# Kernel optimization log

Measured on AMD Instinct MI355X. Metric: run time of the kernel, lower is better.

## Reference

```python
import jax, jax.numpy as jnp
import numpy as np

B, S = 2, 1024
ENC_IN, MARK_IN = 21, 4
PRED_LEN, C_OUT = 96, 21
E = 512                 # embedding_dim
INNER = 2 * E           # proj_factor=2.0 (library default; Model does not pass it)
NH = 8                  # mLSTM heads
DH = INNER // NH        # 128
K = 4                   # causal conv1d kernel
BS = 4                  # qkv_proj_blocksize
NHP = INNER // BS       # 256 block-diagonal proj heads
NB = 4                  # num_blocks
EPS = 1e-5


def setup_inputs() -> dict:
    key = jax.random.key(0)
    ks = jax.random.split(key, 24)
    it = iter(range(24))
    def n(shape, s=0.02):
        return jax.random.normal(ks[next(it)], shape, jnp.float32) * s
    return {
        "x_enc": n((B, S, ENC_IN), 1.0),
        "x_mark_enc": n((B, S, MARK_IN), 1.0),
        "x_dec": n((B, PRED_LEN, ENC_IN), 1.0),
        "x_mark_dec": n((B, PRED_LEN, MARK_IN), 1.0),
        "emb_W": n((ENC_IN + MARK_IN, E), 0.05),
        "emb_b": jnp.zeros((E,), jnp.float32),
        "ln_w": jnp.ones((NB, E), jnp.float32),
        "up_W": n((NB, E, 2 * INNER)),
        "conv_W": n((NB, INNER, K), 0.1),
        "conv_b": jnp.zeros((NB, INNER), jnp.float32),
        "q_W": n((NB, NHP, BS, BS), 0.1),
        "k_W": n((NB, NHP, BS, BS), 0.1),
        "v_W": n((NB, NHP, BS, BS), 0.1),
        "ig_W": n((NB, 3 * INNER, NH)),
        "ig_b": jnp.zeros((NB, NH), jnp.float32),
        "fg_W": n((NB, 3 * INNER, NH)),
        "fg_b": jnp.tile(jnp.linspace(3.0, 6.0, NH, dtype=jnp.float32), (NB, 1)),
        "skip": jnp.ones((NB, INNER), jnp.float32),
        "onorm_w": jnp.ones((NB, INNER), jnp.float32),
        "down_W": n((NB, INNER, E)),
        "post_ln_w": jnp.ones((E,), jnp.float32),
        "head_W": n((E, C_OUT), 0.05),
        "head_b": jnp.zeros((C_OUT,), jnp.float32),
    }


def _ln(x, w):
    mu = jnp.mean(x, -1, keepdims=True)
    var = jnp.var(x, -1, keepdims=True)
    return (x - mu) * jax.lax.rsqrt(var + EPS) * w


def _headwise(x, w):
    # block-diagonal LinearHeadwiseExpand: (B,S,INNER) with (NHP,BS,BS) blocks
    xh = x.reshape(x.shape[0], x.shape[1], NHP, BS)
    return jnp.einsum('bshd,hod->bsho', xh, w).reshape(x.shape)


def _block(x, lw, uW, cW, cb, qW, kW, vW, igW, igb, fgW, fgb, sk, ow, dW):
    xn = _ln(x, lw)
    up = xn @ uW                                  # (B,S,2*INNER)
    xm, z = up[..., :INNER], up[..., INNER:]
    # causal depthwise conv1d + SiLU
    xc = jax.lax.conv_general_dilated(
        xm.transpose(0, 2, 1), cW[:, None, :], (1,), [(K - 1, 0)],
        feature_group_count=INNER,
        dimension_numbers=('NCH', 'OIH', 'NCH')).transpose(0, 2, 1) + cb
    xc = jax.nn.silu(xc)
    q = _headwise(xc, qW)
    k = _headwise(xc, kW)
    v = _headwise(xm, vW)
    qkv = jnp.concatenate([q, k, v], -1)          # (B,S,3*INNER)
    ig = (qkv @ igW + igb).transpose(0, 2, 1)     # (B,NH,S)
    fg = (qkv @ fgW + fgb).transpose(0, 2, 1)
    qh = q.reshape(B, S, NH, DH).transpose(0, 2, 1, 3)
    kh = k.reshape(B, S, NH, DH).transpose(0, 2, 1, 3)
    vh = v.reshape(B, S, NH, DH).transpose(0, 2, 1, 3)
    # parallel stabilized mLSTM (exp-gated linear attention)
    log_f = jax.nn.log_sigmoid(fg)
    cs = jnp.cumsum(log_f, -1)                    # (B,NH,S)
    Mmat = cs[..., :, None] - cs[..., None, :]    # (B,NH,S,S) cumulative decay
    tri = jnp.tril(jnp.ones((S, S), bool))
    logD = jnp.where(tri, Mmat + ig[..., None, :], -jnp.inf)
    m = jnp.max(logD, -1, keepdims=True)          # row-wise stabilizer
    D = jnp.exp(logD - m)
    qk = jnp.einsum('bnsd,bntd->bnst', qh, kh) / (DH ** 0.5)
    C = qk * D
    norm = jnp.maximum(jnp.abs(jnp.sum(C, -1, keepdims=True)), jnp.exp(-m))
    h = jnp.einsum('bnst,bntd->bnsd', C / (norm + 1e-6), vh)
    # multi-head layernorm (groupnorm over DH per head), weight, no bias
    hn = (h - jnp.mean(h, -1, keepdims=True)) * jax.lax.rsqrt(jnp.var(h, -1, keepdims=True) + EPS)
    hn = hn.transpose(0, 2, 1, 3).reshape(B, S, INNER) * ow
    hs = (hn + sk * xc) * jax.nn.silu(z)          # learnable skip + output gate
    return x + hs @ dW                            # residual


def reference(x_enc, x_mark_enc, x_dec, x_mark_dec, emb_W, emb_b, ln_w, up_W,
              conv_W, conv_b, q_W, k_W, v_W, ig_W, ig_b, fg_W, fg_b, skip,
              onorm_w, down_W, post_ln_w, head_W, head_b):
    x = jnp.concatenate([x_enc, x_mark_enc], -1) @ emb_W + emb_b
    for i in range(NB):
        x = _block(x, ln_w[i], up_W[i], conv_W[i], conv_b[i], q_W[i], k_W[i],
                   v_W[i], ig_W[i], ig_b[i], fg_W[i], fg_b[i], skip[i],
                   onorm_w[i], down_W[i])
    x = _ln(x, post_ln_w)
    return x[:, -PRED_LEN:, :] @ head_W + head_b
```

## Files before the change

### kernel.cpp

```cpp
#include <hip/hip_runtime.h>
#include <hip/hip_bf16.h>

#define S_LEN 1024
#define E_DIM 512
#define INNER_D 1024
#define NHEAD 8
#define DHEAD 128

typedef unsigned short u16;
typedef unsigned int u32;
typedef __attribute__((ext_vector_type(8))) short short8;
typedef __attribute__((ext_vector_type(4))) float f32x4;

union S8 { short8 v; u16 u[8]; uint4 q; };

__device__ __forceinline__ u16 f2bf(float f) {
  u32 u = __float_as_uint(f);
  u32 r = u + 0x7FFFu + ((u >> 16) & 1u);
  return (u16)(r >> 16);
}
__device__ __forceinline__ float bf2f(u16 u) { return __uint_as_float(((u32)u) << 16); }

__device__ __forceinline__ void gload16(const u16* g, u16* l) {
  __builtin_amdgcn_global_load_lds((const __attribute__((address_space(1))) void*)g,
                                   (__attribute__((address_space(3))) void*)l, 16, 0, 0);
}

__global__ __launch_bounds__(128) void embed_kernel(
    const float* __restrict__ xe, const float* __restrict__ xm,
    const float* __restrict__ W, const float* __restrict__ bias,
    float* __restrict__ x)
{
  int row = blockIdx.x;
  int tid = threadIdx.x;
  __shared__ float in_s[25];
  if (tid < 21) in_s[tid] = xe[row * 21 + tid];
  else if (tid < 25) in_s[tid] = xm[row * 4 + tid - 21];
  __syncthreads();
#pragma unroll
  for (int rep = 0; rep < 4; rep++) {
    int e = tid + rep * 128;
    float acc = bias[e];
#pragma unroll
    for (int i = 0; i < 25; i++) acc += in_s[i] * W[i * E_DIM + e];
    x[(size_t)row * E_DIM + e] = acc;
  }
}

__global__ __launch_bounds__(256) void ln_kernel(
    const float* __restrict__ x, const float* __restrict__ w, u16* __restrict__ out)
{
  int row = blockIdx.x, tid = threadIdx.x;
  const float* xr = x + (size_t)row * E_DIM;
  float2 v = *(const float2*)(xr + tid * 2);
  float s = v.x + v.y, q = v.x * v.x + v.y * v.y;
#pragma unroll
  for (int off = 32; off; off >>= 1) { s += __shfl_xor(s, off); q += __shfl_xor(q, off); }
  __shared__ float ssum[4], ssq[4];
  int wv = tid >> 6;
  if ((tid & 63) == 0) { ssum[wv] = s; ssq[wv] = q; }
  __syncthreads();
  s = ssum[0] + ssum[1] + ssum[2] + ssum[3];
  q = ssq[0] + ssq[1] + ssq[2] + ssq[3];
  float mu = s * (1.f / E_DIM);
  float var = q * (1.f / E_DIM) - mu * mu;
  float rs = rsqrtf(var + 1e-5f);
  int e = tid * 2;
  ushort2 o;
  o.x = f2bf((v.x - mu) * rs * w[e]);
  o.y = f2bf((v.y - mu) * rs * w[e + 1]);
  *(ushort2*)(out + (size_t)row * E_DIM + e) = o;
}

__global__ __launch_bounds__(256) void lnhead_kernel(
    const float* __restrict__ x, const float* __restrict__ w,
    const float* __restrict__ hW, const float* __restrict__ hb,
    float* __restrict__ out)
{
  int ridx = blockIdx.x;
  int b = ridx / 96, r = ridx % 96;
  int row = b * S_LEN + (S_LEN - 96) + r;
  int tid = threadIdx.x;
  const float* xr = x + (size_t)row * E_DIM;
  float2 v = *(const float2*)(xr + tid * 2);
  float s = v.x + v.y, q = v.x * v.x + v.y * v.y;
#pragma unroll
  for (int off = 32; off; off >>= 1) { s += __shfl_xor(s, off); q += __shfl_xor(q, off); }
  __shared__ float ssum[4], ssq[4];
  __shared__ float lnv[512];
  __shared__ float part[8][32];
  int wv = tid >> 6;
  if ((tid & 63) == 0) { ssum[wv] = s; ssq[wv] = q; }
  __syncthreads();
  s = ssum[0] + ssum[1] + ssum[2] + ssum[3];
  q = ssq[0] + ssq[1] + ssq[2] + ssq[3];
  float mu = s * (1.f / E_DIM);
  float var = q * (1.f / E_DIM) - mu * mu;
  float rs = rsqrtf(var + 1e-5f);
  int e = tid * 2;
  lnv[e]     = (v.x - mu) * rs * w[e];
  lnv[e + 1] = (v.y - mu) * rs * w[e + 1];
  __syncthreads();
  int n = tid & 31, sl = tid >> 5;
  float p = 0.f;
  if (n < 21) {
#pragma unroll 8
    for (int kk = 0; kk < 64; kk++)
      p += lnv[sl * 64 + kk] * hW[(sl * 64 + kk) * 21 + n];
  }
  part[sl][n] = p;
  __syncthreads();
  if (tid < 21) {
    float acc = hb[tid];
#pragma unroll
    for (int j = 0; j < 8; j++) acc += part[j][tid];
    out[ridx * 21 + tid] = acc;
  }
}

__global__ __launch_bounds__(256) void transpose_bf16_all_kernel(
    const float* __restrict__ in0, u16* __restrict__ out0, int K, int N)
{
  __shared__ u16 T[64][72];
  int L = blockIdx.z;
  const float* in = in0 + (size_t)L * K * N;
  u16* out = out0 + (size_t)L * N * K;
  int k0 = blockIdx.x * 64, n0 = blockIdx.y * 64;
  int t = threadIdx.x;
  int kr = t >> 2, nseg = (t & 3) * 16;
  const float* src = in + (size_t)(k0 + kr) * N + n0 + nseg;
#pragma unroll
  for (int j = 0; j < 16; j++) T[kr][nseg + j] = f2bf(src[j]);
  __syncthreads();
  int nr = t >> 2, kseg = (t & 3) * 16;
  u32 u[8];
#pragma unroll
  for (int rr = 0; rr < 8; rr++) {
    u32 lo = T[kseg + 2 * rr][nr];
    u32 hi = T[kseg + 2 * rr + 1][nr];
    u[rr] = lo | (hi << 16);
  }
  u16* dst = out + (size_t)(n0 + nr) * K + k0 + kseg;
  uint4 w0 = {u[0], u[1], u[2], u[3]};
  uint4 w1 = {u[4], u[5], u[6], u[7]};
  *(uint4*)dst = w0;
  *(uint4*)(dst + 8) = w1;
}

__global__ __launch_bounds__(256) void gates_w_transpose_kernel(
    const float* __restrict__ igW, const float* __restrict__ fgW,
    u16* __restrict__ hi, u16* __restrict__ lo)
{
  int L = blockIdx.z;
  int n = blockIdx.y;
  int k = blockIdx.x * 256 + threadIdx.x;
  const float* W = ((n < 8) ? igW : fgW) + (size_t)L * 24576;
  float v = W[(size_t)k * 8 + (n & 7)];
  u16 h = f2bf(v);
  u16 l = f2bf(v - bf2f(h));
  size_t o = ((size_t)L * 16 + n) * 3072 + k;
  hi[o] = h;
  lo[o] = l;
}

__global__ __launch_bounds__(256) void gemm_bf16_split64(
    const u16* __restrict__ A, const u16* __restrict__ Bt,
    float* __restrict__ C0, u16* __restrict__ C1,
    int M, int N, int K, int split_col, int ldc)
{
  __shared__ u16 As0[64 * 64], As1[64 * 64];
  __shared__ u16 Bs0[128 * 64], Bs1[128 * 64];
  const int tid = threadIdx.x;
  const int row0 = blockIdx.y * 64, col0 = blockIdx.x * 128;
  const int wave = tid >> 6, lane = tid & 63;
  const int wr = wave >> 1, wc = wave & 1;
  const int lm = lane & 15, lq = lane >> 4;
  const int lr = lane >> 3;
  const int cg = (lane & 7) ^ lr;
  f32x4 acc[2][4] = {};
  const u16* Abase = A + (size_t)(row0 + lr) * K + cg * 8;
  const u16* Bbase = Bt + (size_t)(col0 + lr) * K + cg * 8;
  const int key = lm & 7;

#define STAGE_UP(AS, BS, K0) do { \
  _Pragma("unroll") for (int i = 0; i < 2; i++) \
    gload16(Abase + (size_t)((wave * 2 + i) * 8) * K + (K0), &AS[(wave * 2 + i) * 512]); \
  _Pragma("unroll") for (int j = 0; j < 4; j++) \
    gload16(Bbase + (size_t)((wave * 4 + j) * 8) * K + (K0), &BS[(wave * 4 + j) * 512]); \
} while (0)

#define COMPUTE_UP(AS, BS) do { \
  short8 af[2][2], bfv[2][4]; \
  _Pragma("unroll") for (int kc = 0; kc < 2; kc++) { \
    _Pragma("unroll") for (int i = 0; i < 2; i++) \
      af[kc][i] = *(const short8*)&AS[(wr * 32 + i * 16 + lm) * 64 + (((kc * 4 + lq) ^ key) * 8)]; \
    _Pragma("unroll") for (int j = 0; j < 4; j++) \
      bfv[kc][j] = *(const short8*)&BS[(wc * 64 + j * 16 + lm) * 64 + (((kc * 4 + lq) ^ key) * 8)]; \
  } \
  _Pragma("unroll") for (int kc = 0; kc < 2; kc++) \
    _Pragma("unroll") for (int i = 0; i < 2; i++) \
      _Pragma("unroll") for (int j = 0; j < 4; j++) \
        acc[i][j] = __builtin_amdgcn_mfma_f32_16x16x32_bf16(af[kc][i], bfv[kc][j], acc[i][j], 0, 0, 0); \
} while (0)

  STAGE_UP(As0, Bs0, 0);
  STAGE_UP(As1, Bs1, 64);
#pragma unroll
  for (int t = 0; t < 8; t++) {
    if (t < 7) asm volatile("s_waitcnt vmcnt(6)" ::: "memory");
    else       asm volatile("s_waitcnt vmcnt(0)" ::: "memory");
    __builtin_amdgcn_sched_barrier(0);
    __builtin_amdgcn_s_barrier();
    if (t & 1) COMPUTE_UP(As1, Bs1); else COMPUTE_UP(As0, Bs0);
    __builtin_amdgcn_s_barrier();
    if (t + 2 < 8) {
      if (t & 1) STAGE_UP(As1, Bs1, (t + 2) * 64);
      else       STAGE_UP(As0, Bs0, (t + 2) * 64);
    }
  }
#undef STAGE_UP
#undef COMPUTE_UP

  const bool toC1 = (col0 >= split_col);
#pragma unroll
  for (int i = 0; i < 2; i++) {
#pragma unroll
    for (int j = 0; j < 4; j++) {
      int col = col0 - (toC1 ? split_col : 0) + wc * 64 + j * 16 + lm;
#pragma unroll
      for (int r = 0; r < 4; r++) {
        int row = row0 + wr * 32 + i * 16 + lq * 4 + r;
        if (toC1) C1[(size_t)row * ldc + col] = f2bf(acc[i][j][r]);
        else C0[(size_t)row * ldc + col] = acc[i][j][r];
      }
    }
  }
}

__global__ __launch_bounds__(256) void gemm_bf16_32(
    const u16* __restrict__ A, const u16* __restrict__ Bt,
    float* __restrict__ C, int M, int N, int K, int ldc)
{
  __shared__ u16 As0[64 * 64], As1[64 * 64];
  __shared__ u16 Bs0[64 * 64], Bs1[64 * 64];
  const int tid = threadIdx.x;
  const int row0 = blockIdx.y * 64, col0 = blockIdx.x * 64;
  const int wave = tid >> 6, lane = tid & 63;
  const int wr = wave >> 1, wc = wave & 1;
  const int lm = lane & 15, lq = lane >> 4;
  const int lr = lane >> 3;
  const int cg = (lane & 7) ^ lr;
  f32x4 acc[2][2] = {};
  const u16* Abase = A + (size_t)(row0 + lr) * K + cg * 8;
  const u16* Bbase = Bt + (size_t)(col0 + lr) * K + cg * 8;
  const int key = lm & 7;

#define STAGE_DN(AS, BS, K0) do { \
  _Pragma("unroll") for (int i = 0; i < 2; i++) \
    gload16(Abase + (size_t)((wave * 2 + i) * 8) * K + (K0), &AS[(wave * 2 + i) * 512]); \
  _Pragma("unroll") for (int j = 0; j < 2; j++) \
    gload16(Bbase + (size_t)((wave * 2 + j) * 8) * K + (K0), &BS[(wave * 2 + j) * 512]); \
} while (0)

#define COMPUTE_DN(AS, BS) do { \
  short8 af[2][2], bfv[2][2]; \
  _Pragma("unroll") for (int kc = 0; kc < 2; kc++) { \
    _Pragma("unroll") for (int i = 0; i < 2; i++) \
      af[kc][i] = *(const short8*)&AS[(wr * 32 + i * 16 + lm) * 64 + (((kc * 4 + lq) ^ key) * 8)]; \
    _Pragma("unroll") for (int j = 0; j < 2; j++) \
      bfv[kc][j] = *(const short8*)&BS[(wc * 32 + j * 16 + lm) * 64 + (((kc * 4 + lq) ^ key) * 8)]; \
  } \
  _Pragma("unroll") for (int kc = 0; kc < 2; kc++) \
    _Pragma("unroll") for (int i = 0; i < 2; i++) \
      _Pragma("unroll") for (int j = 0; j < 2; j++) \
        acc[i][j] = __builtin_amdgcn_mfma_f32_16x16x32_bf16(af[kc][i], bfv[kc][j], acc[i][j], 0, 0, 0); \
} while (0)

  STAGE_DN(As0, Bs0, 0);
  STAGE_DN(As1, Bs1, 64);
#pragma unroll
  for (int t = 0; t < 16; t++) {
    if (t < 15) asm volatile("s_waitcnt vmcnt(4)" ::: "memory");
    else        asm volatile("s_waitcnt vmcnt(0)" ::: "memory");
    __builtin_amdgcn_sched_barrier(0);
    __builtin_amdgcn_s_barrier();
    if (t & 1) COMPUTE_DN(As1, Bs1); else COMPUTE_DN(As0, Bs0);
    __builtin_amdgcn_s_barrier();
    if (t + 2 < 16) {
      if (t & 1) STAGE_DN(As1, Bs1, (t + 2) * 64);
      else       STAGE_DN(As0, Bs0, (t + 2) * 64);
    }
  }
#undef STAGE_DN
#undef COMPUTE_DN

#pragma unroll
  for (int i = 0; i < 2; i++) {
#pragma unroll
    for (int j = 0; j < 2; j++) {
      int col = col0 + wc * 32 + j * 16 + lm;
#pragma unroll
      for (int r = 0; r < 4; r++) {
        int row = row0 + wr * 32 + i * 16 + lq * 4 + r;
        C[(size_t)row * ldc + col] += acc[i][j][r];
      }
    }
  }
}

__global__ __launch_bounds__(256) void convqkv_kernel(
    const float* __restrict__ xm,
    const float* __restrict__ cw, const float* __restrict__ cb,
    const float* __restrict__ qw, const float* __restrict__ kw, const float* __restrict__ vw,
    float* __restrict__ xc, u16* __restrict__ q, u16* __restrict__ k, u16* __restrict__ v)
{
  int r0 = blockIdx.x * 8;
  int s0 = r0 & (S_LEN - 1);
  int g = threadIdx.x;
  int c0 = g * 4;
  const float* base = xm + (size_t)r0 * INNER_D + c0;

  float4 xv[11];
#pragma unroll
  for (int j = 0; j < 11; j++) {
    int ts = s0 - 3 + j;
    float4 t = {0.f, 0.f, 0.f, 0.f};
    if (ts >= 0) t = *(const float4*)(base + (ptrdiff_t)(j - 3) * INNER_D);
    xv[j] = t;
  }
  float cwv[4][4];
#pragma unroll
  for (int c = 0; c < 4; c++)
#pragma unroll
    for (int kk = 0; kk < 4; kk++) cwv[c][kk] = cw[(c0 + c) * 4 + kk];
  float cbv[4] = {cb[c0], cb[c0 + 1], cb[c0 + 2], cb[c0 + 3]};
  const float* qg = qw + g * 16;
  const float* kg = kw + g * 16;
  const float* vg = vw + g * 16;
  float qwv[16], kwv[16], vwv[16];
#pragma unroll
  for (int i = 0; i < 16; i++) { qwv[i] = qg[i]; kwv[i] = kg[i]; vwv[i] = vg[i]; }

#pragma unroll
  for (int i = 0; i < 8; i++) {
    float a0 = cbv[0], a1 = cbv[1], a2 = cbv[2], a3 = cbv[3];
#pragma unroll
    for (int kk = 0; kk < 4; kk++) {
      float4 xvv = xv[i + kk];
      a0 += xvv.x * cwv[0][kk];
      a1 += xvv.y * cwv[1][kk];
      a2 += xvv.z * cwv[2][kk];
      a3 += xvv.w * cwv[3][kk];
    }
    a0 = a0 / (1.f + __expf(-a0));
    a1 = a1 / (1.f + __expf(-a1));
    a2 = a2 / (1.f + __expf(-a2));
    a3 = a3 / (1.f + __expf(-a3));
    float4 accv = {a0, a1, a2, a3};
    *(float4*)(xc + (size_t)(r0 + i) * INNER_D + c0) = accv;

    float xcv[4] = {a0, a1, a2, a3};
    float xmv[4] = {xv[i + 3].x, xv[i + 3].y, xv[i + 3].z, xv[i + 3].w};
    ushort4 qs, ks, vs;
    u16* qp = (u16*)&qs; u16* kp = (u16*)&ks; u16* vp = (u16*)&vs;
#pragma unroll
    for (int o = 0; o < 4; o++) {
      float aq = 0.f, ak = 0.f, av = 0.f;
#pragma unroll
      for (int d = 0; d < 4; d++) {
        aq += xcv[d] * qwv[o * 4 + d];
        ak += xcv[d] * kwv[o * 4 + d];
        av += xmv[d] * vwv[o * 4 + d];
      }
      qp[o] = f2bf(aq); kp[o] = f2bf(ak); vp[o] = f2bf(av);
    }
    size_t off = (size_t)(r0 + i) * INNER_D + c0;
    *(ushort4*)(q + off) = qs;
    *(ushort4*)(k + off) = ks;
    *(ushort4*)(v + off) = vs;
  }
}

__global__ __launch_bounds__(256) void gates_mfma_kernel(
    const u16* __restrict__ q, const u16* __restrict__ k, const u16* __restrict__ v,
    const u16* __restrict__ whi, const u16* __restrict__ wlo,
    const float* __restrict__ igb, const float* __restrict__ fgb,
    float* __restrict__ ig, float* __restrict__ fg)
{
  const int blk = blockIdx.x;
  const int tid = threadIdx.x;
  const int wave = tid >> 6, lane = tid & 63;
  const int lm = lane & 15, lq = lane >> 4;
  const int grow = blk * 16 + lm;
  const u16* parts[3] = {q, k, v};
  f32x4 acc = {};
#pragma unroll 4
  for (int kc = 0; kc < 24; kc++) {
    int k0 = wave * 768 + kc * 32;
    int part = k0 >> 10;
    int idx = (k0 & 1023) + lq * 8;
    S8 a, bh_, bl_;
    a.q = *(const uint4*)(parts[part] + (size_t)grow * INNER_D + idx);
    bh_.q = *(const uint4*)(whi + (size_t)lm * 3072 + k0 + lq * 8);
    bl_.q = *(const uint4*)(wlo + (size_t)lm * 3072 + k0 + lq * 8);
    __builtin_amdgcn_s_setprio(1);
    acc = __builtin_amdgcn_mfma_f32_16x16x32_bf16(a.v, bh_.v, acc, 0, 0, 0);
    acc = __builtin_amdgcn_mfma_f32_16x16x32_bf16(a.v, bl_.v, acc, 0, 0, 0);
    __builtin_amdgcn_s_setprio(0);
  }
  __shared__ float red[4][16][17];
#pragma unroll
  for (int r = 0; r < 4; r++) red[wave][lq * 4 + r][lm] = acc[r];
  __syncthreads();
  if (wave == 0) {
#pragma unroll
    for (int r = 0; r < 4; r++) {
      int row = lq * 4 + r;
      float sum = red[0][row][lm] + red[1][row][lm] + red[2][row][lm] + red[3][row][lm];
      int growr = blk * 16 + row;
      int b = growr >> 10, s = growr & (S_LEN - 1);
      if (lm < 8) ig[((size_t)(b * NHEAD + lm) << 10) + s] = sum + igb[lm];
      else        fg[((size_t)(b * NHEAD + (lm - 8)) << 10) + s] = sum + fgb[lm - 8];
    }
  }
}

__global__ __launch_bounds__(1024) void scan_kernel(
    const float* __restrict__ ig, const float* __restrict__ fg,
    float* __restrict__ a, float* __restrict__ rm, float* __restrict__ enm)
{
  int bh = blockIdx.x;
  int t = threadIdx.x;
  int lane = t & 63, wv = t >> 6;
  __shared__ float sw[16];
  size_t o = ((size_t)bh << 10) + t;
  float f = fg[o];
  float lf = (f >= 0.f) ? -log1pf(__expf(-f)) : f - log1pf(__expf(f));
  float v = lf;
#pragma unroll
  for (int off = 1; off < 64; off <<= 1) {
    float u = __shfl_up(v, off);
    if (lane >= off) v += u;
  }
  if (lane == 63) sw[wv] = v;
  __syncthreads();
  float pre = 0.f;
  for (int w = 0; w < wv; w++) pre += sw[w];
  float cs = v + pre;
  float av = ig[o] - cs;
  a[o] = av;
  float m = av;
#pragma unroll
  for (int off = 1; off < 64; off <<= 1) {
    float u = __shfl_up(m, off);
    if (lane >= off) m = fmaxf(m, u);
  }
  __syncthreads();
  if (lane == 63) sw[wv] = m;
  __syncthreads();
  float pm = -3.4e38f;
  for (int w = 0; w < wv; w++) pm = fmaxf(pm, sw[w]);
  float rmx = fmaxf(m, pm);
  rm[o] = rmx;
  enm[o] = __expf(-(cs + rmx));
}

__device__ __constant__ int c_qt[24] = {7,15,14,15, 6,13,14,12,13, 5,11,12,10,11, 4, 9,10, 8, 9, 3, 8, 2, 1, 0};
__device__ __constant__ int c_k0[24] = {0, 0, 7, 8, 0, 0, 0, 6, 7, 0, 0, 0, 5, 6, 0, 0, 0, 4, 5, 0, 0, 0, 0, 0};
__device__ __constant__ int c_k1[24] = {8, 8,15,16, 7, 7, 7,13,14, 6, 6, 6,11,12, 5, 5, 5, 9,10, 4, 4, 3, 2, 1};
__device__ __constant__ int c_md[24] = {0, 1, 2, 2, 0, 1, 1, 2, 2, 0, 1, 1, 2, 2, 0, 1, 1, 2, 2, 0, 1, 0, 0, 0};

__global__ __launch_bounds__(256) void attn_mfma_kernel(
    const u16* __restrict__ qhg, const u16* __restrict__ khg, const u16* __restrict__ vhg,
    const float* __restrict__ a_arr, const float* __restrict__ rm_arr, const float* __restrict__ enm_arr,
    const float* __restrict__ xc, const u16* __restrict__ zh,
    const float* __restrict__ skip, const float* __restrict__ onw,
    u16* __restrict__ hs, float* __restrict__ hpart, float* __restrict__ scpart)
{
  const int bh = blockIdx.x;
  const int job = blockIdx.y;
  const int qt = c_qt[job], k0t = c_k0[job], k1t = c_k1[job], mode = c_md[job];
  const int b = bh >> 3, h = bh & 7;
  const int s0 = qt * 64;
  const int tid = threadIdx.x;
  const int wave = tid >> 6, lane = tid & 63;
  const int lm = lane & 15, lq = lane >> 4;
  const size_t rowbase = (size_t)b * S_LEN;
  const int c0 = h * DHEAD;

  __shared__ u16 Ks0[64 * 128], Ks1[64 * 128];
  __shared__ u16 Vt0[128 * 72], Vt1[128 * 72];
  __shared__ u16 Ws[64 * 72];
  __shared__ float as0[64], as1[64];

  short8 aq[4];
  {
    const u16* qp = qhg + (rowbase + s0 + wave * 16 + lm) * INNER_D + c0 + lq * 8;
#pragma unroll
    for (int kc = 0; kc < 4; kc++) {
      S8 tmp; tmp.q = *(const uint4*)(qp + kc * 32);
      aq[kc] = tmp.v;
    }
  }
  float rmv[4];
#pragma unroll
  for (int r = 0; r < 4; r++)
    rmv[r] = rm_arr[(size_t)bh * S_LEN + s0 + wave * 16 + lq * 4 + r];

  f32x4 accH[8] = {};
  float sc_acc[4] = {0.f, 0.f, 0.f, 0.f};
  const float scale = 0.08838834764831845f;
  const int lr16 = lane >> 4;
  const int ls16 = lane & 15;
  const int tp0 = tid & 31, dg0 = tid >> 5;
  const int dg1 = dg0 + 8;

  S8 vA0, vA1, vB0, vB1;
  float aval;

#define PREF_K(KS, T0) do { \
  _Pragma("unroll") for (int j = 0; j < 4; j++) { \
    int rK = (wave * 4 + j) * 4 + lr16; \
    int cgk = ls16 ^ (rK & 7); \
    gload16(khg + (rowbase + (T0) + rK) * INNER_D + c0 + cgk * 8, &KS[(wave * 4 + j) * 512]); \
  } \
} while (0)

#define PREF_V(T0) do { \
  const u16* sv = vhg + (rowbase + (T0) + 2 * tp0) * INNER_D + c0 + dg0 * 8; \
  vA0.q = *(const uint4*)sv; \
  vA1.q = *(const uint4*)(sv + INNER_D); \
  const u16* sw2 = vhg + (rowbase + (T0) + 2 * tp0) * INNER_D + c0 + dg1 * 8; \
  vB0.q = *(const uint4*)sw2; \
  vB1.q = *(const uint4*)(sw2 + INNER_D); \
  aval = (tid < 64) ? a_arr[(size_t)bh * S_LEN + (T0) + tid] : 0.f; \
} while (0)

#define WRITE_V(VT, ASB) do { \
  _Pragma("unroll") for (int j = 0; j < 8; j++) \
    *(u32*)&VT[(dg0 * 8 + j) * 72 + 2 * tp0] = (u32)vA0.u[j] | ((u32)vA1.u[j] << 16); \
  _Pragma("unroll") for (int j = 0; j < 8; j++) \
    *(u32*)&VT[(dg1 * 8 + j) * 72 + 2 * tp0] = (u32)vB0.u[j] | ((u32)vB1.u[j] << 16); \
  if (tid < 64) ASB[tid] = aval; \
} while (0)

#define QK_STEP(KS, PACC) do { \
  __builtin_amdgcn_s_setprio(1); \
  _Pragma("unroll") for (int kc = 0; kc < 4; kc++) \
    _Pragma("unroll") for (int cb = 0; cb < 4; cb++) { \
      short8 bk = *(const short8*)&KS[(cb * 16 + lm) * 128 + (((kc * 4 + lq) ^ (lm & 7)) * 8)]; \
      PACC[cb] = __builtin_amdgcn_mfma_f32_16x16x32_bf16(aq[kc], bk, PACC[cb], 0, 0, 0); \
    } \
  __builtin_amdgcn_s_setprio(0); \
} while (0)

#define W_PV(ASB, VT, T0, PACC) do { \
  float wpart[4] = {0.f, 0.f, 0.f, 0.f}; \
  _Pragma("unroll") for (int cb = 0; cb < 4; cb++) { \
    int colg = (T0) + cb * 16 + lm; \
    float ea = ASB[cb * 16 + lm]; \
    _Pragma("unroll") for (int r = 0; r < 4; r++) { \
      int rowg = s0 + wave * 16 + lq * 4 + r; \
      float wv = PACC[cb][r] * scale * __expf(ea - rmv[r]); \
      if (colg > rowg) wv = 0.f; \
      wpart[r] += wv; \
      Ws[(wave * 16 + lq * 4 + r) * 72 + cb * 16 + lm] = f2bf(wv); \
    } \
  } \
  _Pragma("unroll") for (int r = 0; r < 4; r++) { \
    float sr = wpart[r]; \
    sr += __shfl_xor(sr, 1); sr += __shfl_xor(sr, 2); \
    sr += __shfl_xor(sr, 4); sr += __shfl_xor(sr, 8); \
    sc_acc[r] += sr; \
  } \
  __builtin_amdgcn_s_setprio(1); \
  _Pragma("unroll") for (int kc = 0; kc < 2; kc++) { \
    short8 aw = *(const short8*)&Ws[(wave * 16 + lm) * 72 + kc * 32 + lq * 8]; \
    _Pragma("unroll") for (int nb = 0; nb < 8; nb++) { \
      short8 bv = *(const short8*)&VT[(nb * 16 + lm) * 72 + kc * 32 + lq * 8]; \
      accH[nb] = __builtin_amdgcn_mfma_f32_16x16x32_bf16(aw, bv, accH[nb], 0, 0, 0); \
    } \
  } \
  __builtin_amdgcn_s_setprio(0); \
} while (0)

  int kt = k0t;
  PREF_K(Ks0, kt * 64);
  PREF_V(kt * 64);
  WRITE_V(Vt0, as0);
  __syncthreads();

  while (true) {
    {
      bool more = (kt + 1 < k1t);
      if (more) { PREF_K(Ks1, (kt + 1) * 64); PREF_V((kt + 1) * 64); }
      f32x4 pacc[4] = {};
      QK_STEP(Ks0, pacc);
      if (more) WRITE_V(Vt1, as1);
      W_PV(as0, Vt0, kt * 64, pacc);
      __syncthreads();
      kt++;
      if (kt >= k1t) break;
    }
    {
      bool more = (kt + 1 < k1t);
      if (more) { PREF_K(Ks0, (kt + 1) * 64); PREF_V((kt + 1) * 64); }
      f32x4 pacc[4] = {};
      QK_STEP(Ks1, pacc);
      if (more) WRITE_V(Vt0, as0);
      W_PV(as1, Vt1, kt * 64, pacc);
      __syncthreads();
      kt++;
      if (kt >= k1t) break;
    }
  }
#undef PREF_K
#undef PREF_V
#undef WRITE_V
#undef QK_STEP
#undef W_PV

  if (mode != 0) {
    int slot = mode - 1;
    int qr = qt - 8;
    float* Hp = hpart + (((size_t)slot * 16 + bh) * 8 + qr) * 8192;
    float* sp = scpart + ((slot * 16 + bh) * 8 + qr) * 64;
#pragma unroll
    for (int r = 0; r < 4; r++) {
      int row = wave * 16 + lq * 4 + r;
      if (lm == 0) sp[row] = sc_acc[r];
#pragma unroll
      for (int nb = 0; nb < 8; nb++)
        Hp[row * 128 + nb * 16 + lm] = accH[nb][r];
    }
    return;
  }

  float inv[4], muv[4], rsv[4];
#pragma unroll
  for (int r = 0; r < 4; r++) {
    int rowg = s0 + wave * 16 + lq * 4 + r;
    float nrm = fmaxf(fabsf(sc_acc[r]), enm_arr[(size_t)bh * S_LEN + rowg]);
    inv[r] = 1.f / (nrm + 1e-6f);
  }
#pragma unroll
  for (int r = 0; r < 4; r++) {
    float s = 0.f, qq = 0.f;
#pragma unroll
    for (int nb = 0; nb < 8; nb++) {
      float hv = accH[nb][r] * inv[r];
      accH[nb][r] = hv;
      s += hv; qq += hv * hv;
    }
    s += __shfl_xor(s, 1); s += __shfl_xor(s, 2); s += __shfl_xor(s, 4); s += __shfl_xor(s, 8);
    qq += __shfl_xor(qq, 1); qq += __shfl_xor(qq, 2); qq += __shfl_xor(qq, 4); qq += __shfl_xor(qq, 8);
    float mu = s * (1.f / DHEAD);
    float var = qq * (1.f / DHEAD) - mu * mu;
    muv[r] = mu;
    rsv[r] = rsqrtf(var + 1e-5f);
  }
  float ow[8], sk[8];
#pragma unroll
  for (int nb = 0; nb < 8; nb++) {
    ow[nb] = onw[c0 + nb * 16 + lm];
    sk[nb] = skip[c0 + nb * 16 + lm];
  }
#pragma unroll
  for (int r = 0; r < 4; r++) {
    int rowg = s0 + wave * 16 + lq * 4 + r;
    size_t base = (rowbase + rowg) * INNER_D + c0;
#pragma unroll
    for (int nb = 0; nb < 8; nb++) {
      int d = nb * 16 + lm;
      float xcv = xc[base + d];
      float zv = bf2f(zh[base + d]);
      float hn = (accH[nb][r] - muv[r]) * rsv[r] * ow[nb] + sk[nb] * xcv;
      float o = hn * (zv / (1.f + __expf(-zv)));
      hs[base + d] = f2bf(o);
    }
  }
}

__global__ __launch_bounds__(256) void attn_combine_kernel(
    const float* __restrict__ hpart, const float* __restrict__ scpart,
    const float* __restrict__ enm,
    const float* __restrict__ xc, const u16* __restrict__ zh,
    const float* __restrict__ skip, const float* __restrict__ onw,
    u16* __restrict__ hs)
{
  int wave = threadIdx.x >> 6, lane = threadIdx.x & 63;
  int gid = blockIdx.x * 4 + wave;
  int bh = gid >> 9;
  int rr = gid & 511;
  int qr = rr >> 6, row = rr & 63;
  int b = bh >> 3, hh = bh & 7;
  int s = (qr + 8) * 64 + row;
  size_t off = (((size_t)bh) * 8 + qr) * 8192 + row * 128 + lane * 2;
  float2 h0 = *(const float2*)(hpart + off);
  float2 h1 = *(const float2*)(hpart + 1048576 + off);
  int sidx = (bh * 8 + qr) * 64 + row;
  float sc = scpart[sidx] + scpart[8192 + sidx];
  float nrm = fmaxf(fabsf(sc), enm[(size_t)bh * S_LEN + s]);
  float inv = 1.f / (nrm + 1e-6f);
  float hx = (h0.x + h1.x) * inv, hy = (h0.y + h1.y) * inv;
  float sm = hx + hy, sq = hx * hx + hy * hy;
#pragma unroll
  for (int off2 = 32; off2; off2 >>= 1) { sm += __shfl_xor(sm, off2); sq += __shfl_xor(sq, off2); }
  float mu = sm * (1.f / DHEAD);
  float var = sq * (1.f / DHEAD) - mu * mu;
  float rs = rsqrtf(var + 1e-5f);
  int c0 = hh * DHEAD + lane * 2;
  size_t base = ((size_t)(b * S_LEN + s)) * INNER_D + c0;
  float2 xc2 = *(const float2*)(xc + base);
  ushort2 z2u = *(const ushort2*)(zh + base);
  float z2x = bf2f(z2u.x), z2y = bf2f(z2u.y);
  float skx = skip[c0], sky = skip[c0 + 1];
  float owx = onw[c0],  owy = onw[c0 + 1];
  ushort2 o;
  o.x = f2bf(((hx - mu) * rs * owx + skx * xc2.x) * (z2x / (1.f + __expf(-z2x))));
  o.y = f2bf(((hy - mu) * rs * owy + sky * xc2.y) * (z2y / (1.f + __expf(-z2y))));
  *(ushort2*)(hs + base) = o;
}

extern "C" void kernel_launch(void* const* d_in, const int* in_sizes, int n_in,
                              void* d_out, int out_size, void* d_ws, size_t ws_size,
                              hipStream_t stream)
{
  const float* x_enc   = (const float*)d_in[0];
  const float* x_mark  = (const float*)d_in[1];
  const float* emb_W   = (const float*)d_in[4];
  const float* emb_b   = (const float*)d_in[5];
  const float* ln_w    = (const float*)d_in[6];
  const float* up_W    = (const float*)d_in[7];
  const float* conv_W  = (const float*)d_in[8];
  const float* conv_b  = (const float*)d_in[9];
  const float* q_W     = (const float*)d_in[10];
  const float* k_W     = (const float*)d_in[11];
  const float* v_W     = (const float*)d_in[12];
  const float* ig_W    = (const float*)d_in[13];
  const float* ig_b    = (const float*)d_in[14];
  const float* fg_W    = (const float*)d_in[15];
  const float* fg_b    = (const float*)d_in[16];
  const float* skip_w  = (const float*)d_in[17];
  const float* onorm_w = (const float*)d_in[18];
  const float* down_W  = (const float*)d_in[19];
  const float* post_ln = (const float*)d_in[20];
  const float* head_W  = (const float*)d_in[21];
  const float* head_b  = (const float*)d_in[22];

  float* p = (float*)d_ws;
  float* x    = p; p += 1048576;
  float* xm   = p; p += 2097152;
  float* xc   = p; p += 2097152;
  float* igb_ = p; p += 16384;
  float* fgb_ = p; p += 16384;
  float* ab   = p; p += 16384;
  float* rmb  = p; p += 16384;
  float* enmb = p; p += 16384;
  float* ln96 = p; p += 98304;
  u16* qhb = (u16*)p; p += 1048576;
  u16* khb = (u16*)p; p += 1048576;
  u16* vhb = (u16*)p; p += 1048576;
  u16* zh  = (u16*)p; p += 524288;
  u16* xnh = (u16*)p; p += 524288;
  u16* upWtA = (u16*)p; p += 2097152;
  u16* dnWtA = (u16*)p; p += 1048576;
  u16* gtwH = (u16*)p; p += 98304;
  u16* gtwL = (u16*)p; p += 98304;
  float* hpart = p; p += 2097152;
  float* scpart = p; p += 16384;
  u16* hsbh = (u16*)xm;

  embed_kernel<<<2048, 128, 0, stream>>>(x_enc, x_mark, emb_W, emb_b, x);
  transpose_bf16_all_kernel<<<dim3(8, 32, 4), 256, 0, stream>>>(up_W, upWtA, 512, 2048);
  transpose_bf16_all_kernel<<<dim3(16, 8, 4), 256, 0, stream>>>(down_W, dnWtA, 1024, 512);
  gates_w_transpose_kernel<<<dim3(12, 16, 4), 256, 0, stream>>>(ig_W, fg_W, gtwH, gtwL);

  for (int L = 0; L < 4; L++) {
    ln_kernel<<<2048, 256, 0, stream>>>(x, ln_w + L * 512, xnh);
    gemm_bf16_split64<<<dim3(16, 32), 256, 0, stream>>>(
        xnh, upWtA + (size_t)L * 1048576, xm, zh, 2048, 2048, 512, 1024, 1024);
    convqkv_kernel<<<256, 256, 0, stream>>>(
        xm, conv_W + L * 4096, conv_b + L * 1024,
        q_W + L * 4096, k_W + L * 4096, v_W + L * 4096,
        xc, qhb, khb, vhb);
    gates_mfma_kernel<<<128, 256, 0, stream>>>(
        qhb, khb, vhb, gtwH + (size_t)L * 49152, gtwL + (size_t)L * 49152,
        ig_b + L * 8, fg_b + L * 8, igb_, fgb_);
    scan_kernel<<<16, 1024, 0, stream>>>(igb_, fgb_, ab, rmb, enmb);
    attn_mfma_kernel<<<dim3(16, 24), 256, 0, stream>>>(
        qhb, khb, vhb, ab, rmb, enmb, xc, zh,
        skip_w + L * 1024, onorm_w + L * 1024, hsbh, hpart, scpart);
    attn_combine_kernel<<<2048, 256, 0, stream>>>(
        hpart, scpart, enmb, xc, zh, skip_w + L * 1024, onorm_w + L * 1024, hsbh);
    gemm_bf16_32<<<dim3(8, 32), 256, 0, stream>>>(
        hsbh, dnWtA + (size_t)L * 524288, x, 2048, 512, 1024, 512);
  }

  lnhead_kernel<<<192, 256, 0, stream>>>(x, post_ln, head_W, head_b, (float*)d_out);
}
```

Before: 472.1 us.

## Pre-transpose V and async-prefetch K/V tiles in attention; retile up-projection GEMM

Adds a kernel that transposes V into a per-batch (channel, time) layout. The attention kernel can then load both K and V tiles straight into LDS with async global-to-LDS loads, replacing the register-staged V transpose and shared-memory gate copy. The K loop becomes a double-buffered prefetch pipeline with explicit vmcnt waits and barriers. Separately, the up-projection GEMM moves to 128x128 tiles with K-step 32, halving the grid. The costs are an extra launch plus a V round trip through memory, and fewer GEMM blocks for occupancy.

```diff
diff --git a/kernel.cpp b/kernel.cpp
--- a/kernel.cpp
+++ b/kernel.cpp
@@ -147,6 +147,37 @@
   *(uint4*)(dst + 8) = w1;
 }
 
+__global__ __launch_bounds__(256) void vtrans_kernel(
+    const u16* __restrict__ v, u16* __restrict__ vt)
+{
+  __shared__ u16 T[64][72];
+  int r0 = blockIdx.x * 64;
+  int d0 = blockIdx.y * 64;
+  int t = threadIdx.x;
+  int sr = t >> 2, dseg = (t & 3) * 16;
+  const u16* src = v + (size_t)(r0 + sr) * INNER_D + d0 + dseg;
+  S8 a0, a1;
+  a0.q = *(const uint4*)src;
+  a1.q = *(const uint4*)(src + 8);
+#pragma unroll
+  for (int j = 0; j < 8; j++) { T[sr][dseg + j] = a0.u[j]; T[sr][dseg + 8 + j] = a1.u[j]; }
+  __syncthreads();
+  int dr = t >> 2, sseg = (t & 3) * 16;
+  u32 u[8];
+#pragma unroll
+  for (int rr = 0; rr < 8; rr++) {
+    u32 lo = T[sseg + 2 * rr][dr];
+    u32 hi = T[sseg + 2 * rr + 1][dr];
+    u[rr] = lo | (hi << 16);
+  }
+  int b = r0 >> 10;
+  u16* dst = vt + ((size_t)b * INNER_D + d0 + dr) * S_LEN + (r0 & (S_LEN - 1)) + sseg;
+  uint4 w0 = {u[0], u[1], u[2], u[3]};
+  uint4 w1 = {u[4], u[5], u[6], u[7]};
+  *(uint4*)dst = w0;
+  *(uint4*)(dst + 8) = w1;
+}
+
 __global__ __launch_bounds__(256) void gates_w_transpose_kernel(
     const float* __restrict__ igW, const float* __restrict__ fgW,
     u16* __restrict__ hi, u16* __restrict__ lo)
@@ -168,68 +199,66 @@
     float* __restrict__ C0, u16* __restrict__ C1,
     int M, int N, int K, int split_col, int ldc)
 {
-  __shared__ u16 As0[64 * 64], As1[64 * 64];
-  __shared__ u16 Bs0[128 * 64], Bs1[128 * 64];
+  __shared__ u16 As0[128 * 32], As1[128 * 32];
+  __shared__ u16 Bs0[128 * 32], Bs1[128 * 32];
   const int tid = threadIdx.x;
-  const int row0 = blockIdx.y * 64, col0 = blockIdx.x * 128;
+  const int row0 = blockIdx.y * 128, col0 = blockIdx.x * 128;
   const int wave = tid >> 6, lane = tid & 63;
   const int wr = wave >> 1, wc = wave & 1;
   const int lm = lane & 15, lq = lane >> 4;
-  const int lr = lane >> 3;
-  const int cg = (lane & 7) ^ lr;
-  f32x4 acc[2][4] = {};
-  const u16* Abase = A + (size_t)(row0 + lr) * K + cg * 8;
-  const u16* Bbase = Bt + (size_t)(col0 + lr) * K + cg * 8;
-  const int key = lm & 7;
-
-#define STAGE_UP(AS, BS, K0) do { \
+  const int lr4 = lane >> 2;
+  const int cg4 = (lane & 3) ^ (lr4 & 3);
+  f32x4 acc[4][4] = {};
+  const u16* Abase = A + (size_t)(row0 + lr4) * K + cg4 * 8;
+  const u16* Bbase = Bt + (size_t)(col0 + lr4) * K + cg4 * 8;
+  const int key = lm & 3;
+
+#define STG_UP(AS, BS, K0) do { \
   _Pragma("unroll") for (int i = 0; i < 2; i++) \
-    gload16(Abase + (size_t)((wave * 2 + i) * 8) * K + (K0), &AS[(wave * 2 + i) * 512]); \
+    gload16(Abase + (size_t)((wave * 2 + i) * 16) * K + (K0), &AS[(wave * 2 + i) * 512]); \
+  _Pragma("unroll") for (int i = 0; i < 2; i++) \
+    gload16(Bbase + (size_t)((wave * 2 + i) * 16) * K + (K0), &BS[(wave * 2 + i) * 512]); \
+} while (0)
+
+#define CMP_UP(AS, BS) do { \
+  short8 af[4], bfv[4]; \
+  _Pragma("unroll") for (int i = 0; i < 4; i++) \
+    af[i] = *(const short8*)&AS[(wr * 64 + i * 16 + lm) * 32 + ((lq ^ key) * 8)]; \
   _Pragma("unroll") for (int j = 0; j < 4; j++) \
-    gload16(Bbase + (size_t)((wave * 4 + j) * 8) * K + (K0), &BS[(wave * 4 + j) * 512]); \
+    bfv[j] = *(const short8*)&BS[(wc * 64 + j * 16 + lm) * 32 + ((lq ^ key) * 8)]; \
+  _Pragma("unroll") for (int i = 0; i < 4; i++) \
+    _Pragma("unroll") for (int j = 0; j < 4; j++) \
+      acc[i][j] = __builtin_amdgcn_mfma_f32_16x16x32_bf16(af[i], bfv[j], acc[i][j], 0, 0, 0); \
 } while (0)
 
-#define COMPUTE_UP(AS, BS) do { \
-  short8 af[2][2], bfv[2][4]; \
-  _Pragma("unroll") for (int kc = 0; kc < 2; kc++) { \
-    _Pragma("unroll") for (int i = 0; i < 2; i++) \
-      af[kc][i] = *(const short8*)&AS[(wr * 32 + i * 16 + lm) * 64 + (((kc * 4 + lq) ^ key) * 8)]; \
-    _Pragma("unroll") for (int j = 0; j < 4; j++) \
-      bfv[kc][j] = *(const short8*)&BS[(wc * 64 + j * 16 + lm) * 64 + (((kc * 4 + lq) ^ key) * 8)]; \
-  } \
-  _Pragma("unroll") for (int kc = 0; kc < 2; kc++) \
-    _Pragma("unroll") for (int i = 0; i < 2; i++) \
-      _Pragma("unroll") for (int j = 0; j < 4; j++) \
-        acc[i][j] = __builtin_amdgcn_mfma_f32_16x16x32_bf16(af[kc][i], bfv[kc][j], acc[i][j], 0, 0, 0); \
-} while (0)
-
-  STAGE_UP(As0, Bs0, 0);
-  STAGE_UP(As1, Bs1, 64);
-#pragma unroll
-  for (int t = 0; t < 8; t++) {
-    if (t < 7) asm volatile("s_waitcnt vmcnt(6)" ::: "memory");
-    else       asm volatile("s_waitcnt vmcnt(0)" ::: "memory");
+  STG_UP(As0, Bs0, 0);
+  asm volatile("" ::: "memory");
+  STG_UP(As1, Bs1, 32);
+#pragma unroll
+  for (int t = 0; t < 16; t++) {
+    if (t < 15) asm volatile("s_waitcnt vmcnt(4)" ::: "memory");
+    else        asm volatile("s_waitcnt vmcnt(0)" ::: "memory");
     __builtin_amdgcn_sched_barrier(0);
     __builtin_amdgcn_s_barrier();
-    if (t & 1) COMPUTE_UP(As1, Bs1); else COMPUTE_UP(As0, Bs0);
+    if (t & 1) CMP_UP(As1, Bs1); else CMP_UP(As0, Bs0);
     __builtin_amdgcn_s_barrier();
-    if (t + 2 < 8) {
-      if (t & 1) STAGE_UP(As1, Bs1, (t + 2) * 64);
-      else       STAGE_UP(As0, Bs0, (t + 2) * 64);
-    }
-  }
-#undef STAGE_UP
-#undef COMPUTE_UP
+    if (t + 2 < 16) {
+      if (t & 1) STG_UP(As1, Bs1, (t + 2) * 32);
+      else       STG_UP(As0, Bs0, (t + 2) * 32);
+    }
+  }
+#undef STG_UP
+#undef CMP_UP
 
   const bool toC1 = (col0 >= split_col);
 #pragma unroll
-  for (int i = 0; i < 2; i++) {
+  for (int i = 0; i < 4; i++) {
 #pragma unroll
     for (int j = 0; j < 4; j++) {
       int col = col0 - (toC1 ? split_col : 0) + wc * 64 + j * 16 + lm;
 #pragma unroll
       for (int r = 0; r < 4; r++) {
-        int row = row0 + wr * 32 + i * 16 + lq * 4 + r;
+        int row = row0 + wr * 64 + i * 16 + lq * 4 + r;
         if (toC1) C1[(size_t)row * ldc + col] = f2bf(acc[i][j][r]);
         else C0[(size_t)row * ldc + col] = acc[i][j][r];
       }
@@ -277,6 +306,7 @@
 } while (0)
 
   STAGE_DN(As0, Bs0, 0);
+  asm volatile("" ::: "memory");
   STAGE_DN(As1, Bs1, 64);
 #pragma unroll
   for (int t = 0; t < 16; t++) {
@@ -471,7 +501,7 @@
 __device__ __constant__ int c_md[24] = {0, 1, 2, 2, 0, 1, 1, 2, 2, 0, 1, 1, 2, 2, 0, 1, 1, 2, 2, 0, 1, 0, 0, 0};
 
 __global__ __launch_bounds__(256) void attn_mfma_kernel(
-    const u16* __restrict__ qhg, const u16* __restrict__ khg, const u16* __restrict__ vhg,
+    const u16* __restrict__ qhg, const u16* __restrict__ khg, const u16* __restrict__ vtg,
     const float* __restrict__ a_arr, const float* __restrict__ rm_arr, const float* __restrict__ enm_arr,
     const float* __restrict__ xc, const u16* __restrict__ zh,
     const float* __restrict__ skip, const float* __restrict__ onw,
@@ -489,9 +519,8 @@
   const int c0 = h * DHEAD;
 
   __shared__ u16 Ks0[64 * 128], Ks1[64 * 128];
-  __shared__ u16 Vt0[128 * 72], Vt1[128 * 72];
+  __shared__ u16 Vt0[128 * 64], Vt1[128 * 64];
   __shared__ u16 Ws[64 * 72];
-  __shared__ float as0[64], as1[64];
 
   short8 aq[4];
   {
@@ -512,36 +541,24 @@
   const float scale = 0.08838834764831845f;
   const int lr16 = lane >> 4;
   const int ls16 = lane & 15;
-  const int tp0 = tid & 31, dg0 = tid >> 5;
-  const int dg1 = dg0 + 8;
-
-  S8 vA0, vA1, vB0, vB1;
-  float aval;
-
-#define PREF_K(KS, T0) do { \
+  const int lr8 = lane >> 3;
+  const int cgv = (lane & 7) ^ lr8;
+  const u16* vtbase = vtg + ((size_t)b * INNER_D + c0) * S_LEN;
+
+  float ae0[4], ae1[4];
+
+#define PREF(KS, VS, AE, T0) do { \
   _Pragma("unroll") for (int j = 0; j < 4; j++) { \
     int rK = (wave * 4 + j) * 4 + lr16; \
     int cgk = ls16 ^ (rK & 7); \
     gload16(khg + (rowbase + (T0) + rK) * INNER_D + c0 + cgk * 8, &KS[(wave * 4 + j) * 512]); \
   } \
-} while (0)
-
-#define PREF_V(T0) do { \
-  const u16* sv = vhg + (rowbase + (T0) + 2 * tp0) * INNER_D + c0 + dg0 * 8; \
-  vA0.q = *(const uint4*)sv; \
-  vA1.q = *(const uint4*)(sv + INNER_D); \
-  const u16* sw2 = vhg + (rowbase + (T0) + 2 * tp0) * INNER_D + c0 + dg1 * 8; \
-  vB0.q = *(const uint4*)sw2; \
-  vB1.q = *(const uint4*)(sw2 + INNER_D); \
-  aval = (tid < 64) ? a_arr[(size_t)bh * S_LEN + (T0) + tid] : 0.f; \
-} while (0)
-
-#define WRITE_V(VT, ASB) do { \
-  _Pragma("unroll") for (int j = 0; j < 8; j++) \
-    *(u32*)&VT[(dg0 * 8 + j) * 72 + 2 * tp0] = (u32)vA0.u[j] | ((u32)vA1.u[j] << 16); \
-  _Pragma("unroll") for (int j = 0; j < 8; j++) \
-    *(u32*)&VT[(dg1 * 8 + j) * 72 + 2 * tp0] = (u32)vB0.u[j] | ((u32)vB1.u[j] << 16); \
-  if (tid < 64) ASB[tid] = aval; \
+  _Pragma("unroll") for (int j = 0; j < 4; j++) { \
+    int rV = (wave * 4 + j) * 8 + lr8; \
+    gload16(vtbase + (size_t)rV * S_LEN + (T0) + cgv * 8, &VS[(wave * 4 + j) * 512]); \
+  } \
+  _Pragma("unroll") for (int cb = 0; cb < 4; cb++) \
+    AE[cb] = a_arr[(size_t)bh * S_LEN + (T0) + cb * 16 + lm]; \
 } while (0)
 
 #define QK_STEP(KS, PACC) do { \
@@ -554,11 +571,11 @@
   __builtin_amdgcn_s_setprio(0); \
 } while (0)
 
-#define W_PV(ASB, VT, T0, PACC) do { \
+#define W_PV(AE, VT, T0, PACC) do { \
   float wpart[4] = {0.f, 0.f, 0.f, 0.f}; \
   _Pragma("unroll") for (int cb = 0; cb < 4; cb++) { \
     int colg = (T0) + cb * 16 + lm; \
-    float ea = ASB[cb * 16 + lm]; \
+    float ea = AE[cb]; \
     _Pragma("unroll") for (int r = 0; r < 4; r++) { \
       int rowg = s0 + wave * 16 + lq * 4 + r; \
       float wv = PACC[cb][r] * scale * __expf(ea - rmv[r]); \
@@ -577,7 +594,7 @@
   _Pragma("unroll") for (int kc = 0; kc < 2; kc++) { \
     short8 aw = *(const short8*)&Ws[(wave * 16 + lm) * 72 + kc * 32 + lq * 8]; \
     _Pragma("unroll") for (int nb = 0; nb < 8; nb++) { \
-      short8 bv = *(const short8*)&VT[(nb * 16 + lm) * 72 + kc * 32 + lq * 8]; \
+      short8 bv = *(const short8*)&VT[(nb * 16 + lm) * 64 + (((kc * 4 + lq) ^ (lm & 7)) * 8)]; \
       accH[nb] = __builtin_amdgcn_mfma_f32_16x16x32_bf16(aw, bv, accH[nb], 0, 0, 0); \
     } \
   } \
@@ -585,38 +602,39 @@
 } while (0)
 
   int kt = k0t;
-  PREF_K(Ks0, kt * 64);
-  PREF_V(kt * 64);
-  WRITE_V(Vt0, as0);
-  __syncthreads();
+  PREF(Ks0, Vt0, ae0, kt * 64);
+  asm volatile("" ::: "memory");
+  if (kt + 1 < k1t) PREF(Ks1, Vt1, ae1, (kt + 1) * 64);
 
   while (true) {
     {
-      bool more = (kt + 1 < k1t);
-      if (more) { PREF_K(Ks1, (kt + 1) * 64); PREF_V((kt + 1) * 64); }
+      if (kt + 1 < k1t) asm volatile("s_waitcnt vmcnt(12)" ::: "memory");
+      else              asm volatile("s_waitcnt vmcnt(0)" ::: "memory");
+      __builtin_amdgcn_sched_barrier(0);
+      __builtin_amdgcn_s_barrier();
       f32x4 pacc[4] = {};
       QK_STEP(Ks0, pacc);
-      if (more) WRITE_V(Vt1, as1);
-      W_PV(as0, Vt0, kt * 64, pacc);
-      __syncthreads();
+      W_PV(ae0, Vt0, kt * 64, pacc);
+      __builtin_amdgcn_s_barrier();
+      if (kt + 2 < k1t) PREF(Ks0, Vt0, ae0, (kt + 2) * 64);
       kt++;
       if (kt >= k1t) break;
     }
     {
-      bool more = (kt + 1 < k1t);
-      if (more) { PREF_K(Ks0, (kt + 1) * 64); PREF_V((kt + 1) * 64); }
+      if (kt + 1 < k1t) asm volatile("s_waitcnt vmcnt(12)" ::: "memory");
+      else              asm volatile("s_waitcnt vmcnt(0)" ::: "memory");
+      __builtin_amdgcn_sched_barrier(0);
+      __builtin_amdgcn_s_barrier();
       f32x4 pacc[4] = {};
       QK_STEP(Ks1, pacc);
-      if (more) WRITE_V(Vt0, as0);
-      W_PV(as1, Vt1, kt * 64, pacc);
-      __syncthreads();
+      W_PV(ae1, Vt1, kt * 64, pacc);
+      __builtin_amdgcn_s_barrier();
+      if (kt + 2 < k1t) PREF(Ks1, Vt1, ae1, (kt + 2) * 64);
       kt++;
       if (kt >= k1t) break;
     }
   }
-#undef PREF_K
-#undef PREF_V
-#undef WRITE_V
+#undef PREF
 #undef QK_STEP
 #undef W_PV
 
@@ -769,6 +787,7 @@
   u16* gtwL = (u16*)p; p += 98304;
   float* hpart = p; p += 2097152;
   float* scpart = p; p += 16384;
+  u16* vtg = (u16*)p; p += 1048576;
   u16* hsbh = (u16*)xm;
 
   embed_kernel<<<2048, 128, 0, stream>>>(x_enc, x_mark, emb_W, emb_b, x);
@@ -778,18 +797,19 @@
 
   for (int L = 0; L < 4; L++) {
     ln_kernel<<<2048, 256, 0, stream>>>(x, ln_w + L * 512, xnh);
-    gemm_bf16_split64<<<dim3(16, 32), 256, 0, stream>>>(
+    gemm_bf16_split64<<<dim3(16, 16), 256, 0, stream>>>(
         xnh, upWtA + (size_t)L * 1048576, xm, zh, 2048, 2048, 512, 1024, 1024);
     convqkv_kernel<<<256, 256, 0, stream>>>(
         xm, conv_W + L * 4096, conv_b + L * 1024,
         q_W + L * 4096, k_W + L * 4096, v_W + L * 4096,
         xc, qhb, khb, vhb);
+    vtrans_kernel<<<dim3(32, 16), 256, 0, stream>>>(vhb, vtg);
     gates_mfma_kernel<<<128, 256, 0, stream>>>(
         qhb, khb, vhb, gtwH + (size_t)L * 49152, gtwL + (size_t)L * 49152,
         ig_b + L * 8, fg_b + L * 8, igb_, fgb_);
     scan_kernel<<<16, 1024, 0, stream>>>(igb_, fgb_, ab, rmb, enmb);
     attn_mfma_kernel<<<dim3(16, 24), 256, 0, stream>>>(
-        qhb, khb, vhb, ab, rmb, enmb, xc, zh,
+        qhb, khb, vtg, ab, rmb, enmb, xc, zh,
         skip_w + L * 1024, onorm_w + L * 1024, hsbh, hpart, scpart);
     attn_combine_kernel<<<2048, 256, 0, stream>>>(
         hpart, scpart, enmb, xc, zh, skip_w + L * 1024, onorm_w + L * 1024, hsbh);
```

After: 464.7 us. No clear change (-1.6%).
